# Optimization experiments

Hardware: AMD Instinct MI355X
Metric: run time of the kernel (lower is better)

The kernel has to match this reference:

```python
import jax, jax.numpy as jnp
import numpy as np
import math

D_MODEL = 4096
NUM_HEADS = 32
NUM_KV_HEADS = 8
HEAD_DIM = D_MODEL // NUM_HEADS  # 128
GROUP = NUM_HEADS // NUM_KV_HEADS  # 4
SEQ_LEN = 2048
BATCH = 2
ROPE_THETA = 10000.0


def apply_rope(x, start_pos=0):
    # x: [b, h, s, hd]; llama-style rotation on interleaved (even, odd) pairs
    b, h, s, hd = x.shape
    inv_freq = 1.0 / (ROPE_THETA ** (jnp.arange(0, hd, 2, dtype=jnp.float32) / hd))  # [hd/2]
    pos = jnp.arange(start_pos, start_pos + s, dtype=jnp.float32)  # [s]
    ang = pos[:, None] * inv_freq[None, :]  # [s, hd/2]
    cos = jnp.cos(ang).astype(x.dtype)
    sin = jnp.sin(ang).astype(x.dtype)
    xr = x[..., 0::2]  # [b,h,s,hd/2]
    xi = x[..., 1::2]
    out_r = xr * cos - xi * sin
    out_i = xr * sin + xi * cos
    return jnp.stack([out_r, out_i], axis=-1).reshape(b, h, s, hd)


def setup_inputs() -> dict:
    key = jax.random.key(0)
    ks = jax.random.split(key, 5)
    qkv_dim = HEAD_DIM * (NUM_HEADS + 2 * NUM_KV_HEADS)  # 6144
    scale = 1.0 / math.sqrt(D_MODEL)
    return {
        "x": jax.random.normal(ks[0], (BATCH, SEQ_LEN, D_MODEL), jnp.float32),
        "w_qkv": jax.random.normal(ks[1], (qkv_dim, D_MODEL), jnp.float32) * scale,
        "b_qkv": jax.random.normal(ks[2], (qkv_dim,), jnp.float32) * 0.01,
        "w_o": jax.random.normal(ks[3], (D_MODEL, D_MODEL), jnp.float32) * scale,
        "b_o": jax.random.normal(ks[4], (D_MODEL,), jnp.float32) * 0.01,
    }


def reference(x, w_qkv, b_qkv, w_o, b_o):
    bs, seq_len, d_model = x.shape
    qkv = x @ w_qkv.T + b_qkv  # [b, s, 6144]
    q_dim = NUM_HEADS * HEAD_DIM
    kv_dim = NUM_KV_HEADS * HEAD_DIM
    q, k, v = jnp.split(qkv, [q_dim, q_dim + kv_dim], axis=-1)
    q = q.reshape(bs, seq_len, NUM_HEADS, HEAD_DIM).transpose(0, 2, 1, 3)
    k = k.reshape(bs, seq_len, NUM_KV_HEADS, HEAD_DIM).transpose(0, 2, 1, 3)
    v = v.reshape(bs, seq_len, NUM_KV_HEADS, HEAD_DIM).transpose(0, 2, 1, 3)
    q = apply_rope(q, 0)
    k = apply_rope(k, 0)
    # repeat_kv: kv head i -> q heads [i*group, (i+1)*group)
    k = jnp.repeat(k, GROUP, axis=1)  # [b, H, s, hd]
    v = jnp.repeat(v, GROUP, axis=1)
    scores = jnp.einsum("bhqd,bhkd->bhqk", q, k) / math.sqrt(HEAD_DIM)
    causal = jnp.tril(jnp.ones((seq_len, seq_len), dtype=bool))
    scores = jnp.where(causal[None, None, :, :], scores, jnp.float32(-1e20))
    attn = jax.nn.softmax(scores, axis=-1)
    out = jnp.einsum("bhqk,bhkd->bhqd", attn, v)
    out = out.transpose(0, 2, 1, 3).reshape(bs, seq_len, d_model)
    return out @ w_o.T + b_o
```

## Files before the change

### kernel.cpp

```cpp
#include <hip/hip_runtime.h>

typedef unsigned short u16;
typedef unsigned int   u32;

#define BATCH   2
#define SEQ     2048
#define DMODEL  4096
#define NHEADS  32
#define NKV     8
#define HDIM    128
#define QKV_DIM 6144

typedef __bf16 bf16x8 __attribute__((ext_vector_type(8)));
typedef float  f32x4  __attribute__((ext_vector_type(4)));

__device__ __forceinline__ float b2f(u16 u) {
  u32 x = ((u32)u) << 16;
  return __builtin_bit_cast(float, x);
}
__device__ __forceinline__ u16 f2b(float f) {
  u32 x = __builtin_bit_cast(u32, f);
  x = (x + 0x7FFFu + ((x >> 16) & 1u)) >> 16;
  return (u16)x;
}
__device__ __forceinline__ float b2f_lo(u32 p) { return __builtin_bit_cast(float, p << 16); }
__device__ __forceinline__ float b2f_hi(u32 p) { return __builtin_bit_cast(float, p & 0xFFFF0000u); }

__device__ __forceinline__ u32 pk(float a, float b) {
  return (u32)f2b(a) | ((u32)f2b(b) << 16);
}

__device__ __forceinline__ void gload16(const u16* __restrict__ g, u16* l) {
  __builtin_amdgcn_global_load_lds(
      (const __attribute__((address_space(1))) unsigned int*)(const void*)g,
      (__attribute__((address_space(3))) unsigned int*)(void*)l,
      16, 0, 0);
}

__global__ __launch_bounds__(256) void f32_to_bf16(const float* __restrict__ in,
                                                   u16* __restrict__ out, int n8) {
  const int i = blockIdx.x * 256 + threadIdx.x;
  if (i >= n8) return;
  const float4* p = (const float4*)(in + (size_t)i * 8);
  const float4 a = p[0], b = p[1];
  uint4 r;
  r.x = pk(a.x, a.y); r.y = pk(a.z, a.w); r.z = pk(b.x, b.y); r.w = pk(b.z, b.w);
  ((uint4*)out)[i] = r;
}

template <int MODE>
__global__ __launch_bounds__(512) void gemm_bt3(const u16* __restrict__ Ab,
                                                const u16* __restrict__ Bw,
                                                const float* __restrict__ bias,
                                                float* __restrict__ outf,
                                                u16* __restrict__ oq,
                                                u16* __restrict__ ok,
                                                u16* __restrict__ ov,
                                                int K, int N) {
  __shared__ u16 As[2][256 * 64];
  __shared__ u16 Bs[2][256 * 64];
  const int t    = threadIdx.x;
  const int lane = t & 63;
  const int wv   = t >> 6;
  const int wr   = wv >> 2, wc = wv & 3;
  const int q4   = lane >> 4, l15 = lane & 15;

  const int nwgx = gridDim.x;
  const int nwg  = nwgx * gridDim.y;
  int bid = blockIdx.y * nwgx + blockIdx.x;
  const int cpx = nwg >> 3;
  bid = (bid & 7) * cpx + (bid >> 3);
  const int m0 = (bid / nwgx) * 256, n0 = (bid % nwgx) * 256;

  f32x4 acc[8][4] = {};

  auto STAGE = [&](int buf, int k0) {
#pragma unroll
    for (int i = 0; i < 4; i++) {
      const int u = t + i * 512;
      const int r = u >> 3, c8 = (u & 7) * 8;
      gload16(Bw + (size_t)(n0 + r) * K + k0 + c8, &Bs[buf][u * 8]);
    }
#pragma unroll
    for (int i = 0; i < 4; i++) {
      const int u = t + i * 512;
      const int r = u >> 3, c8 = (u & 7) * 8;
      gload16(Ab + (size_t)(m0 + r) * K + k0 + c8, &As[buf][u * 8]);
    }
  };

  auto COMPUTE = [&](int buf) {
#pragma unroll
    for (int kk = 0; kk < 2; kk++) {
      bf16x8 af[8], bfr[4];
#pragma unroll
      for (int i = 0; i < 8; i++)
        af[i] = *(const bf16x8*)&As[buf][(wr * 128 + i * 16 + l15) * 64 + kk * 32 + q4 * 8];
#pragma unroll
      for (int j = 0; j < 4; j++)
        bfr[j] = *(const bf16x8*)&Bs[buf][(wc * 64 + j * 16 + l15) * 64 + kk * 32 + q4 * 8];
#pragma unroll
      for (int i = 0; i < 8; i++)
#pragma unroll
        for (int j = 0; j < 4; j++)
          acc[i][j] = __builtin_amdgcn_mfma_f32_16x16x32_bf16(af[i], bfr[j], acc[i][j], 0, 0, 0);
    }
  };

  STAGE(0, 0);
  __syncthreads();

  int cur = 0;
  for (int k0 = 64; k0 < K; k0 += 64) {
    STAGE(cur ^ 1, k0);
    COMPUTE(cur);
    __syncthreads();
    cur ^= 1;
  }
  COMPUTE(cur);

#pragma unroll
  for (int j = 0; j < 4; j++) {
    const int gn = n0 + wc * 64 + j * 16 + l15;
    const float bv = bias[gn];
#pragma unroll
    for (int i = 0; i < 8; i++) {
      const int gmb = m0 + wr * 128 + i * 16 + q4 * 4;
#pragma unroll
      for (int rr = 0; rr < 4; rr++) {
        float val = acc[i][j][rr] + bv;
        const int gm = gmb + rr;
        if (MODE == 1) {
          outf[(size_t)gm * N + gn] = val;
        } else {
          const int b = gm >> 11, s = gm & (SEQ - 1);
          const int d = gn & (HDIM - 1);
          if (gn < 4096) {
            val *= 0.08838834764831845f;
            const int hh = gn >> 7;
            oq[((size_t)(b * NHEADS + hh) * SEQ + s) * HDIM + d] = f2b(val);
          } else if (gn < 5120) {
            const int hh = (gn - 4096) >> 7;
            ok[((size_t)(b * NKV + hh) * SEQ + s) * HDIM + d] = f2b(val);
          } else {
            const int hh = (gn - 5120) >> 7;
            ov[((size_t)(b * NKV + hh) * SEQ + s) * HDIM + d] = f2b(val);
          }
        }
      }
    }
  }
}

__global__ __launch_bounds__(256) void rope_kernel(u16* __restrict__ q, u16* __restrict__ kk,
                                                   int qrows, int totrows) {
  const int idx = blockIdx.x * 256 + threadIdx.x;
  const int row = idx >> 6;
  const int i   = idx & 63;
  if (row >= totrows) return;
  u16* base;
  int r;
  if (row < qrows) { base = q  + (size_t)row * HDIM;           r = row; }
  else             { base = kk + (size_t)(row - qrows) * HDIM; r = row - qrows; }
  const int s = r & (SEQ - 1);
  const float l2theta = 13.287712379549449f;
  const float inv = exp2f(-((float)(2 * i) * (1.0f / 128.0f)) * l2theta);
  const float ang = (float)s * inv;
  const float c  = cosf(ang);
  const float sn = sinf(ang);
  const u32 xv = *(const u32*)&base[2 * i];
  const float xr = b2f_lo(xv), xi = b2f_hi(xv);
  *(u32*)&base[2 * i] = pk(xr * c - xi * sn, xr * sn + xi * c);
}

__global__ __launch_bounds__(256, 2) void attn_mfma(const u16* __restrict__ q,
                                                    const u16* __restrict__ k,
                                                    const u16* __restrict__ v,
                                                    u16* __restrict__ out) {
  __shared__ u16 Ks[64 * 136];
  __shared__ u16 VtBuf[128 * 72];
  __shared__ u32 Ps32[4 * 32 * 36];
  u32* Vt32 = (u32*)VtBuf;

  const int t    = threadIdx.x;
  const int lane = t & 63;
  const int w    = t >> 6;
  const int q4   = lane >> 4, l15 = lane & 15;
  const int qb   = 15 - (int)blockIdx.x;
  const int h = blockIdx.y, b = blockIdx.z;
  const int m0 = qb * 128;
  const int mw = m0 + w * 32;
  const int kvh = h >> 2;
  const u16* Qp = q + (size_t)(b * NHEADS + h) * SEQ * HDIM;
  const u16* Kp = k + (size_t)(b * NKV + kvh) * SEQ * HDIM;
  const u16* Vp = v + (size_t)(b * NKV + kvh) * SEQ * HDIM;

  bf16x8 qf[2][4];
#pragma unroll
  for (int rt = 0; rt < 2; rt++)
#pragma unroll
    for (int kk = 0; kk < 4; kk++)
      qf[rt][kk] = *(const bf16x8*)&Qp[(size_t)(mw + rt * 16 + l15) * HDIM + kk * 32 + q4 * 8];

  f32x4 oacc[2][8] = {};
  float mrow[2], lrow[2];
  mrow[0] = mrow[1] = -1e30f;
  lrow[0] = lrow[1] = 0.f;

  u32* Pw32 = &Ps32[w * 32 * 36];

  const int nch = qb * 2 + 2;
  for (int kc = 0; kc < nch; kc++) {
#pragma unroll
    for (int i = 0; i < 4; i++) {
      const int u = t + i * 256;
      const int r = u >> 4, c = (u & 15) * 8;
      *(uint4*)&Ks[r * 136 + c] = *(const uint4*)&Kp[(size_t)(kc * 64 + r) * HDIM + c];
    }
    uint2 e0[4], e1[4];
#pragma unroll
    for (int i = 0; i < 4; i++) {
      const int tau = t + i * 256;
      const int k2 = tau >> 5, dq = tau & 31;
      e0[i] = *(const uint2*)&Vp[(size_t)(kc * 64 + 2 * k2) * HDIM + dq * 4];
      e1[i] = *(const uint2*)&Vp[(size_t)(kc * 64 + 2 * k2 + 1) * HDIM + dq * 4];
    }
    __syncthreads();

    const bool part = (kc * 64 <= mw + 31);
    if (part) {
      const bool fullch = (kc * 64 + 63 <= mw);
      f32x4 sacc[2][4] = {};
      __builtin_amdgcn_s_setprio(1);
#pragma unroll
      for (int ct = 0; ct < 4; ct++) {
#pragma unroll
        for (int kk = 0; kk < 4; kk++) {
          const bf16x8 kb = *(const bf16x8*)&Ks[(ct * 16 + l15) * 136 + kk * 32 + q4 * 8];
          sacc[0][ct] = __builtin_amdgcn_mfma_f32_16x16x32_bf16(kb, qf[0][kk], sacc[0][ct], 0, 0, 0);
          sacc[1][ct] = __builtin_amdgcn_mfma_f32_16x16x32_bf16(kb, qf[1][kk], sacc[1][ct], 0, 0, 0);
        }
      }
      __builtin_amdgcn_s_setprio(0);
#pragma unroll
      for (int rt = 0; rt < 2; rt++) {
        float p[4][4];
        float cm[4];
        const int mm = mw + rt * 16 + l15;
#pragma unroll
        for (int ct = 0; ct < 4; ct++) {
#pragma unroll
          for (int rr = 0; rr < 4; rr++) {
            float s = sacc[rt][ct][rr];
            if (!fullch) {
              const int key = kc * 64 + ct * 16 + q4 * 4 + rr;
              s = (key <= mm) ? s : -1e30f;
            }
            p[ct][rr] = s;
          }
          cm[ct] = fmaxf(fmaxf(p[ct][0], p[ct][1]), fmaxf(p[ct][2], p[ct][3]));
        }
        float vmax = fmaxf(fmaxf(cm[0], cm[1]), fmaxf(cm[2], cm[3]));
        vmax = fmaxf(vmax, __shfl_xor(vmax, 16));
        vmax = fmaxf(vmax, __shfl_xor(vmax, 32));
        const float nm = fmaxf(mrow[rt], vmax);
        const float alpha = __expf(mrow[rt] - nm);
        mrow[rt] = nm;
        float cs[4];
#pragma unroll
        for (int ct = 0; ct < 4; ct++) {
#pragma unroll
          for (int rr = 0; rr < 4; rr++) p[ct][rr] = __expf(p[ct][rr] - nm);
          cs[ct] = (p[ct][0] + p[ct][1]) + (p[ct][2] + p[ct][3]);
        }
        lrow[rt] = lrow[rt] * alpha + ((cs[0] + cs[1]) + (cs[2] + cs[3]));
#pragma unroll
        for (int ct = 0; ct < 4; ct++) {
          uint2 w2;
          w2.x = pk(p[ct][0], p[ct][1]);
          w2.y = pk(p[ct][2], p[ct][3]);
          *(uint2*)&Pw32[(rt * 16 + l15) * 36 + ct * 8 + q4 * 2] = w2;
        }
        float alT[4];
#pragma unroll
        for (int rr = 0; rr < 4; rr++) alT[rr] = __shfl(alpha, q4 * 4 + rr, 64);
#pragma unroll
        for (int dt = 0; dt < 8; dt++)
#pragma unroll
          for (int rr = 0; rr < 4; rr++) oacc[rt][dt][rr] *= alT[rr];
      }
    }
#pragma unroll
    for (int i = 0; i < 4; i++) {
      const int tau = t + i * 256;
      const int k2 = tau >> 5, dq = tau & 31;
      u32 wj[4];
      wj[0] = (e0[i].x & 0xFFFFu) | (e1[i].x << 16);
      wj[1] = (e0[i].x >> 16)     | (e1[i].x & 0xFFFF0000u);
      wj[2] = (e0[i].y & 0xFFFFu) | (e1[i].y << 16);
      wj[3] = (e0[i].y >> 16)     | (e1[i].y & 0xFFFF0000u);
      const int g = k2 >> 2;
#pragma unroll
      for (int j = 0; j < 4; j++) {
        const int d = dq * 4 + j;
        const int gs = g ^ ((d >> 3) & 7);
        Vt32[d * 36 + gs * 4 + (k2 & 3)] = wj[j];
      }
    }
    __syncthreads();

    if (part) {
      __builtin_amdgcn_s_setprio(1);
#pragma unroll
      for (int kk2 = 0; kk2 < 2; kk2++) {
        bf16x8 pa[2];
        pa[0] = *(const bf16x8*)&Pw32[(l15) * 36 + kk2 * 16 + q4 * 4];
        pa[1] = *(const bf16x8*)&Pw32[(16 + l15) * 36 + kk2 * 16 + q4 * 4];
#pragma unroll
        for (int dt = 0; dt < 8; dt++) {
          const int d = dt * 16 + l15;
          const int gs = (kk2 * 4 + q4) ^ ((d >> 3) & 7);
          const bf16x8 vb = *(const bf16x8*)&Vt32[d * 36 + gs * 4];
          oacc[0][dt] = __builtin_amdgcn_mfma_f32_16x16x32_bf16(pa[0], vb, oacc[0][dt], 0, 0, 0);
          oacc[1][dt] = __builtin_amdgcn_mfma_f32_16x16x32_bf16(pa[1], vb, oacc[1][dt], 0, 0, 0);
        }
      }
      __builtin_amdgcn_s_setprio(0);
    }
  }

#pragma unroll
  for (int rt = 0; rt < 2; rt++) {
    float ls = lrow[rt];
    ls += __shfl_xor(ls, 16);
    ls += __shfl_xor(ls, 32);
#pragma unroll
    for (int rr = 0; rr < 4; rr++) {
      const float lt = __shfl(ls, q4 * 4 + rr, 64);
      const float inv = 1.0f / lt;
      const int mm = mw + rt * 16 + q4 * 4 + rr;
      u16* op = &out[((size_t)(b * SEQ + mm)) * DMODEL + h * HDIM + l15];
#pragma unroll
      for (int dt = 0; dt < 8; dt++)
        op[dt * 16] = f2b(oacc[rt][dt][rr] * inv);
    }
  }
}

extern "C" void kernel_launch(void* const* d_in, const int* in_sizes, int n_in,
                              void* d_out, int out_size, void* d_ws, size_t ws_size,
                              hipStream_t stream) {
  const float* x     = (const float*)d_in[0];
  const float* w_qkv = (const float*)d_in[1];
  const float* b_qkv = (const float*)d_in[2];
  const float* w_o   = (const float*)d_in[3];
  const float* b_o   = (const float*)d_in[4];
  float* out = (float*)d_out;

  const size_t QN = (size_t)BATCH * NHEADS * SEQ * HDIM;
  const size_t KN = (size_t)BATCH * NKV * SEQ * HDIM;

  u16* q    = (u16*)d_ws;
  u16* k    = q + QN;
  u16* v    = k + KN;
  u16* attn = v + KN;
  u16* wb   = attn + QN;
  u16* xb   = attn;

  const dim3 blk(256);
  const dim3 blk512(512);

  const int n8_x = BATCH * SEQ * DMODEL / 8;
  f32_to_bf16<<<dim3(n8_x / 256), blk, 0, stream>>>(x, xb, n8_x);
  const int n8_qkv = QKV_DIM * DMODEL / 8;
  f32_to_bf16<<<dim3(n8_qkv / 256), blk, 0, stream>>>(w_qkv, wb, n8_qkv);

  gemm_bt3<0><<<dim3(QKV_DIM / 256, (BATCH * SEQ) / 256), blk512, 0, stream>>>(
      xb, wb, b_qkv, nullptr, q, k, v, DMODEL, QKV_DIM);

  const int qrows = BATCH * NHEADS * SEQ;
  const int totrows = qrows + BATCH * NKV * SEQ;
  rope_kernel<<<dim3((totrows * 64) / 256), blk, 0, stream>>>(q, k, qrows, totrows);

  attn_mfma<<<dim3(SEQ / 128, NHEADS, BATCH), blk, 0, stream>>>(q, k, v, attn);

  const int n8_o = DMODEL * DMODEL / 8;
  f32_to_bf16<<<dim3(n8_o / 256), blk, 0, stream>>>(w_o, wb, n8_o);

  gemm_bt3<1><<<dim3(DMODEL / 256, (BATCH * SEQ) / 256), blk512, 0, stream>>>(
      attn, wb, b_o, out, nullptr, nullptr, nullptr, DMODEL, DMODEL);
}
```

Measured before the change: 1.037 ms.

## Restructure GEMM into 4-slot half-tile pipeline with interleaved loads and barriers

Replaces the double-buffered 256x256x64 GEMM main loop with a four-slot ring of 32-wide K half-tiles, prefetching three half-tiles ahead. Each half-tile's MFMA work is split into two phases, with the A and B global-to-LDS loads issued between them. Explicit vmcnt waits, pinned barriers and s_setprio replace the single __syncthreads per iteration. The aim is to overlap memory latency with MFMA work and smooth out issue contention, at the cost of more barriers per K step and fragile hand-tuned wait counts.

```diff
diff --git a/kernel.cpp b/kernel.cpp
--- a/kernel.cpp
+++ b/kernel.cpp
@@ -35,6 +35,12 @@
       (const __attribute__((address_space(1))) unsigned int*)(const void*)g,
       (__attribute__((address_space(3))) unsigned int*)(void*)l,
       16, 0, 0);
+}
+
+__device__ __forceinline__ void barrier_pinned() {
+  __builtin_amdgcn_sched_barrier(0);
+  __builtin_amdgcn_s_barrier();
+  __builtin_amdgcn_sched_barrier(0);
 }
 
 __global__ __launch_bounds__(256) void f32_to_bf16(const float* __restrict__ in,
@@ -48,8 +54,18 @@
   ((uint4*)out)[i] = r;
 }
 
+__device__ __forceinline__ void stage_ht(const u16* __restrict__ gbase, int K,
+                                         u16* __restrict__ dst, int t) {
+#pragma unroll
+  for (int j2 = 0; j2 < 2; j2++) {
+    const int u = t + j2 * 512;
+    const int r = u >> 2, cu = u & 3;
+    gload16(gbase + (size_t)r * K + cu * 8, &dst[u * 8]);
+  }
+}
+
 template <int MODE>
-__global__ __launch_bounds__(512) void gemm_bt3(const u16* __restrict__ Ab,
+__global__ __launch_bounds__(512) void gemm_8ph(const u16* __restrict__ Ab,
                                                 const u16* __restrict__ Bw,
                                                 const float* __restrict__ bias,
                                                 float* __restrict__ outf,
@@ -57,8 +73,8 @@
                                                 u16* __restrict__ ok,
                                                 u16* __restrict__ ov,
                                                 int K, int N) {
-  __shared__ u16 As[2][256 * 64];
-  __shared__ u16 Bs[2][256 * 64];
+  __shared__ u16 As[4][256 * 32];
+  __shared__ u16 Bs[4][256 * 32];
   const int t    = threadIdx.x;
   const int lane = t & 63;
   const int wv   = t >> 6;
@@ -72,52 +88,67 @@
   bid = (bid & 7) * cpx + (bid >> 3);
   const int m0 = (bid / nwgx) * 256, n0 = (bid % nwgx) * 256;
 
+  const u16* Abase = Ab + (size_t)m0 * K;
+  const u16* Bbase = Bw + (size_t)n0 * K;
+  const int NT = K >> 6;
+  const int NHT = 2 * NT;
+
   f32x4 acc[8][4] = {};
 
-  auto STAGE = [&](int buf, int k0) {
-#pragma unroll
-    for (int i = 0; i < 4; i++) {
-      const int u = t + i * 512;
-      const int r = u >> 3, c8 = (u & 7) * 8;
-      gload16(Bw + (size_t)(n0 + r) * K + k0 + c8, &Bs[buf][u * 8]);
-    }
-#pragma unroll
-    for (int i = 0; i < 4; i++) {
-      const int u = t + i * 512;
-      const int r = u >> 3, c8 = (u & 7) * 8;
-      gload16(Ab + (size_t)(m0 + r) * K + k0 + c8, &As[buf][u * 8]);
-    }
-  };
-
-  auto COMPUTE = [&](int buf) {
-#pragma unroll
-    for (int kk = 0; kk < 2; kk++) {
+#pragma unroll
+  for (int m = 0; m < 3; m++) {
+    const int koff = (m >> 1) * 64 + (m & 1) * 32;
+    stage_ht(Abase + koff, K, &As[m & 3][0], t);
+    stage_ht(Bbase + koff, K, &Bs[m & 3][0], t);
+  }
+  asm volatile("s_waitcnt vmcnt(4)" ::: "memory");
+  barrier_pinned();
+
+  for (int kt = 0; kt < NT; kt++) {
+#pragma unroll
+    for (int kh = 0; kh < 2; kh++) {
+      const int g  = 2 * kt + kh;
+      const int sl = g & 3;
+      const u16* Asl = &As[sl][0];
+      const u16* Bsl = &Bs[sl][0];
+
       bf16x8 af[8], bfr[4];
 #pragma unroll
       for (int i = 0; i < 8; i++)
-        af[i] = *(const bf16x8*)&As[buf][(wr * 128 + i * 16 + l15) * 64 + kk * 32 + q4 * 8];
+        af[i] = *(const bf16x8*)&Asl[(wr * 128 + i * 16 + l15) * 32 + q4 * 8];
 #pragma unroll
       for (int j = 0; j < 4; j++)
-        bfr[j] = *(const bf16x8*)&Bs[buf][(wc * 64 + j * 16 + l15) * 64 + kk * 32 + q4 * 8];
-#pragma unroll
-      for (int i = 0; i < 8; i++)
-#pragma unroll
-        for (int j = 0; j < 4; j++)
-          acc[i][j] = __builtin_amdgcn_mfma_f32_16x16x32_bf16(af[i], bfr[j], acc[i][j], 0, 0, 0);
-    }
-  };
-
-  STAGE(0, 0);
-  __syncthreads();
-
-  int cur = 0;
-  for (int k0 = 64; k0 < K; k0 += 64) {
-    STAGE(cur ^ 1, k0);
-    COMPUTE(cur);
-    __syncthreads();
-    cur ^= 1;
-  }
-  COMPUTE(cur);
+        bfr[j] = *(const bf16x8*)&Bsl[(wc * 64 + j * 16 + l15) * 32 + q4 * 8];
+
+      const int ms = g + 3;
+      const int koff = (ms >> 1) * 64 + (ms & 1) * 32;
+      if (ms < NHT) stage_ht(Abase + koff, K, &As[ms & 3][0], t);
+
+      barrier_pinned();
+      __builtin_amdgcn_s_setprio(1);
+#pragma unroll
+      for (int i = 0; i < 8; i++) {
+        acc[i][0] = __builtin_amdgcn_mfma_f32_16x16x32_bf16(af[i], bfr[0], acc[i][0], 0, 0, 0);
+        acc[i][1] = __builtin_amdgcn_mfma_f32_16x16x32_bf16(af[i], bfr[1], acc[i][1], 0, 0, 0);
+      }
+      __builtin_amdgcn_s_setprio(0);
+      barrier_pinned();
+
+      if (ms < NHT) stage_ht(Bbase + koff, K, &Bs[ms & 3][0], t);
+      __builtin_amdgcn_s_setprio(1);
+#pragma unroll
+      for (int i = 0; i < 8; i++) {
+        acc[i][2] = __builtin_amdgcn_mfma_f32_16x16x32_bf16(af[i], bfr[2], acc[i][2], 0, 0, 0);
+        acc[i][3] = __builtin_amdgcn_mfma_f32_16x16x32_bf16(af[i], bfr[3], acc[i][3], 0, 0, 0);
+      }
+      __builtin_amdgcn_s_setprio(0);
+      if (kh == 1) {
+        if (kt < NT - 2)       asm volatile("s_waitcnt vmcnt(4)" ::: "memory");
+        else if (kt == NT - 2) asm volatile("s_waitcnt vmcnt(0)" ::: "memory");
+      }
+      barrier_pinned();
+    }
+  }
 
 #pragma unroll
   for (int j = 0; j < 4; j++) {
@@ -375,7 +406,7 @@
   const int n8_qkv = QKV_DIM * DMODEL / 8;
   f32_to_bf16<<<dim3(n8_qkv / 256), blk, 0, stream>>>(w_qkv, wb, n8_qkv);
 
-  gemm_bt3<0><<<dim3(QKV_DIM / 256, (BATCH * SEQ) / 256), blk512, 0, stream>>>(
+  gemm_8ph<0><<<dim3(QKV_DIM / 256, (BATCH * SEQ) / 256), blk512, 0, stream>>>(
       xb, wb, b_qkv, nullptr, q, k, v, DMODEL, QKV_DIM);
 
   const int qrows = BATCH * NHEADS * SEQ;
@@ -387,6 +418,6 @@
   const int n8_o = DMODEL * DMODEL / 8;
   f32_to_bf16<<<dim3(n8_o / 256), blk, 0, stream>>>(w_o, wb, n8_o);
 
-  gemm_bt3<1><<<dim3(DMODEL / 256, (BATCH * SEQ) / 256), blk512, 0, stream>>>(
+  gemm_8ph<1><<<dim3(DMODEL / 256, (BATCH * SEQ) / 256), blk512, 0, stream>>>(
       attn, wb, b_o, out, nullptr, nullptr, nullptr, DMODEL, DMODEL);
 }
```

Result: faster. 914.5 us (-11.8%).
